# Kernel tuning notes

Hardware: AMD Instinct MI355X
Metric: run time of the kernel (lower is better)

The kernel has to match this reference:

```python
import jax, jax.numpy as jnp
import numpy as np
from jax import lax

N, L, C_IN, NOISE_C, COMP, NC = 256, 512, 514, 112, 16, 2
MAIN_IN = NOISE_C + COMP  # 128
FEAT = NC * 4 * L         # 4096

def _conv1d(x, w, b, pad):
    # x [N,C,L], w [O,I,K]
    y = lax.conv_general_dilated(x, w, (1,), [(pad, pad)], dimension_numbers=('NCH', 'OIH', 'NCH'))
    return y + b[None, :, None]

def _bn(x, g, b):
    # BatchNorm1d, training mode: biased batch stats over (N, L)
    m = x.mean(axis=(0, 2), keepdims=True)
    v = x.var(axis=(0, 2), keepdims=True)
    return (x - m) * lax.rsqrt(v + 1e-5) * g[None, :, None] + b[None, :, None]

def _lrelu(x):
    return jnp.where(x >= 0, x, 0.2 * x)

def _pos_encode(length, dim):
    j = np.arange(dim)
    div = 1.0 / np.power(10000.0, 2 * (j[:, None] // 2) / dim)   # [dim,1]
    ang = np.arange(length)[None, :] * div                       # [dim,length]
    ang = np.where((j % 2 == 0)[:, None], np.sin(ang), np.cos(ang))
    return jnp.asarray(ang[None], jnp.float32)                   # [1,dim,length]

def _assemble(circle_prob, slider_prob):
    # Vectorized run-length label expansion equivalent to the per-sample python while-loop.
    # circle_prob [N, L/2, 2], slider_prob [N, L/4, 2] -> [N, L, 3]
    n, B = slider_prob.shape[0], slider_prob.shape[1]
    c = jnp.argmax(circle_prob, -1)
    s = jnp.argmax(slider_prob, -1)
    zc = jnp.zeros(circle_prob.shape[:-1] + (1,), circle_prob.dtype)
    zs = jnp.zeros(slider_prob.shape[:-1] + (1,), slider_prob.dtype)
    cp3 = jnp.concatenate([circle_prob, zc], -1)                                   # insert 0 at class 2
    sp3 = jnp.concatenate([slider_prob[..., :1], zs, slider_prob[..., 1:]], -1)    # insert 0 at class 1
    pad100 = jnp.array([1., 0., 0.], cp3.dtype)
    pad001 = jnp.array([0., 0., 1.], cp3.dtype)
    bidx = jnp.arange(B)[None, :]
    # slider-body blocks: slider run continues and not cut by sequence end
    body = (s == 1) & (bidx < B - 1)
    prev_body = jnp.concatenate([jnp.zeros((n, 1), bool), body[:, :-1]], 1)
    # tail block ends a slider run (either run stops, or boundary block)
    tail = ((s == 1) & (bidx == B - 1)) | ((s == 0) & prev_body)
    # circle emission for each half-step: prob row if predicted circle else pad
    cr0 = jnp.where((c == 1)[..., None], cp3, pad100).reshape(n, B, 2, 3)
    bodyE = body[..., None]
    row0 = jnp.where((body | tail)[..., None], sp3, cr0[:, :, 0, :])
    row1 = jnp.where(bodyE, pad001, pad100)
    row2 = jnp.where(bodyE, pad001, cr0[:, :, 1, :])
    row3 = jnp.where(bodyE, pad001, pad100)
    return jnp.stack([row0, row1, row2, row3], 2).reshape(n, 4 * B, 3)

def _forward(noise, cond_data, gumbel_u, ext_w1, ext_b1, ext_w2, ext_b2, ext_bn_g, ext_bn_b,
             m_w1, m_b1, m_w2, m_b2, m_bn_g, m_bn_b, lin_w, lin_b, circ_w, circ_b, slid_w, slid_b):
    # FeatureExtractor
    x = cond_data.transpose(0, 2, 1)                      # [N, 514, L]
    x = _lrelu(_conv1d(x, ext_w1, ext_b1, 0))             # [N, 32, L]
    cond = _bn(_conv1d(x, ext_w2, ext_b2, 1), ext_bn_g, ext_bn_b)  # [N, 16, L]
    gen_in = jnp.concatenate([cond, noise.transpose(0, 2, 1)], 1) + _pos_encode(L, MAIN_IN)  # [N,128,L]
    h = _lrelu(_conv1d(gen_in, m_w1, m_b1, 3))            # [N, 32, L]
    h = _lrelu(_bn(_conv1d(h, m_w2, m_b2, 1), m_bn_g, m_bn_b))     # [N, 8, L]
    flat = _lrelu(h.reshape(h.shape[0], -1) @ lin_w + lin_b)       # [N, 4096]
    circle_prob = (flat @ circ_w + circ_b).reshape(-1, L // 2, NC)
    slider_prob = (flat @ slid_w + slid_b).reshape(-1, L // 4, NC)
    out = _assemble(circle_prob, slider_prob)             # [N, L, 3]
    # gumbel_softmax(hard=True, tau=1)
    g = -jnp.log(-jnp.log(gumbel_u + 1e-10) + 1e-10)
    logits = out + g
    y_soft = jax.nn.softmax(logits, -1)
    y_hard = jax.nn.one_hot(jnp.argmax(logits, -1), 3, dtype=y_soft.dtype)
    gen_out = y_hard + y_soft - lax.stop_gradient(y_soft)
    return gen_out, cond

def setup_inputs() -> dict:
    key = jax.random.key(0)
    ks = jax.random.split(key, 12)
    def rn(k, shape, fan_in):
        return jax.random.normal(k, shape, jnp.float32) * (1.0 / fan_in) ** 0.5
    return {
        'noise': jax.random.normal(ks[0], (N, L, NOISE_C), jnp.float32),
        'cond_data': jax.random.normal(ks[1], (N, L, C_IN), jnp.float32),
        'gumbel_u': jax.random.uniform(ks[2], (N, L, 3), jnp.float32),
        'ext_w1': rn(ks[3], (C_IN // 16, C_IN, 1), C_IN), 'ext_b1': jnp.zeros(C_IN // 16),
        'ext_w2': rn(ks[4], (COMP, C_IN // 16, 3), 3 * (C_IN // 16)), 'ext_b2': jnp.zeros(COMP),
        'ext_bn_g': jnp.ones(COMP), 'ext_bn_b': jnp.zeros(COMP),
        'm_w1': rn(ks[5], (NC * 16, MAIN_IN, 7), 7 * MAIN_IN), 'm_b1': jnp.zeros(NC * 16),
        'm_w2': rn(ks[6], (NC * 4, NC * 16, 3), 3 * NC * 16), 'm_b2': jnp.zeros(NC * 4),
        'm_bn_g': jnp.ones(NC * 4), 'm_bn_b': jnp.zeros(NC * 4),
        'lin_w': rn(ks[7], (FEAT, FEAT), FEAT), 'lin_b': jnp.zeros(FEAT),
        'circ_w': rn(ks[8], (FEAT, NC * L // 2), FEAT), 'circ_b': jnp.zeros(NC * L // 2),
        'slid_w': rn(ks[9], (FEAT, NC * L // 4), FEAT), 'slid_b': jnp.zeros(NC * L // 4),
    }

def reference(noise, cond_data, gumbel_u, ext_w1, ext_b1, ext_w2, ext_b2, ext_bn_g, ext_bn_b,
              m_w1, m_b1, m_w2, m_b2, m_bn_g, m_bn_b, lin_w, lin_b, circ_w, circ_b, slid_w, slid_b):
    return _forward(noise, cond_data, gumbel_u, ext_w1, ext_b1, ext_w2, ext_b2, ext_bn_g, ext_bn_b,
                    m_w1, m_b1, m_w2, m_b2, m_bn_g, m_bn_b, lin_w, lin_b, circ_w, circ_b, slid_w, slid_b)
```

## Files before the change

### kernel.cpp

```cpp
#include <hip/hip_runtime.h>
#include <math.h>

#define NB 256
#define LL 512
#define CIN 514

__device__ __forceinline__ float lrelu(float x) { return x >= 0.f ? x : 0.2f * x; }

__global__ __launch_bounds__(256) void k_pos(float* __restrict__ pos) {
    int idx = blockIdx.x * 256 + threadIdx.x;
    int c = idx >> 9, l = idx & 511;
    double e = (double)(2 * (c >> 1)) / 128.0;
    double dv = 1.0 / pow(10000.0, e);
    double a = (double)l * dv;
    pos[idx] = (float)((c & 1) ? cos(a) : sin(a));
}

__global__ __launch_bounds__(256) void k_posconv(const float* __restrict__ POS, const float* __restrict__ W,
                                                 const float* __restrict__ bias, float* __restrict__ PC) {
    const int t = threadIdx.x;
    const int o = blockIdx.x >> 4, l0 = (blockIdx.x & 15) * 32;
    const int l = l0 + (t & 31), cs = t >> 5;
    float acc = 0.f;
    for (int ci = 0; ci < 16; ++ci) {
        int c = cs * 16 + ci;
        float wv[7];
#pragma unroll
        for (int k = 0; k < 7; ++k) wv[k] = W[o * 896 + c * 7 + k];
#pragma unroll
        for (int k = 0; k < 7; ++k) {
            int gl = l + k - 3;
            if (gl >= 0 && gl < LL) acc += wv[k] * POS[c * LL + gl];
        }
    }
    __shared__ float red[8][33];
    red[cs][t & 31] = acc;
    __syncthreads();
    if (cs == 0) {
        float s = bias[o];
#pragma unroll
        for (int j = 0; j < 8; ++j) s += red[j][t & 31];
        PC[o * LL + l0 + (t & 31)] = s;
    }
}

__global__ __launch_bounds__(256) void k_conv1(const float* __restrict__ X, const float* __restrict__ W,
                                               const float* __restrict__ bias, float* __restrict__ out) {
    __shared__ __align__(16) float As[32][260];
    __shared__ __align__(16) float Bs[32][32];
    const int t = threadIdx.x;
    const int pos0 = blockIdx.x * 256;
    const int tx = t & 31, ty = t >> 5;
    const int rl = t >> 4, kp = t & 15;
    float acc[8][4];
#pragma unroll
    for (int p = 0; p < 8; ++p)
#pragma unroll
        for (int q = 0; q < 4; ++q) acc[p][q] = 0.f;

    for (int k0 = 0; k0 < CIN; k0 += 32) {
#pragma unroll
        for (int pass = 0; pass < 16; ++pass) {
            int row = pass * 16 + rl;
            int kk = kp * 2, gk = k0 + kk;
            float vx = 0.f, vy = 0.f;
            if (gk + 1 < CIN) {
                float2 v = *reinterpret_cast<const float2*>(X + (size_t)(pos0 + row) * CIN + gk);
                vx = v.x; vy = v.y;
            } else if (gk < CIN) {
                vx = X[(size_t)(pos0 + row) * CIN + gk];
            }
            As[kk][row] = vx;
            As[kk + 1][row] = vy;
        }
        {
            int o = t & 31, kg = t >> 5;
#pragma unroll
            for (int j = 0; j < 4; ++j) {
                int kk = kg * 4 + j, gk = k0 + kk;
                Bs[kk][o] = (gk < CIN) ? W[o * CIN + gk] : 0.f;
            }
        }
        __syncthreads();
#pragma unroll 8
        for (int kk = 0; kk < 32; ++kk) {
            float4 a0 = *reinterpret_cast<const float4*>(&As[kk][tx * 4]);
            float4 a1 = *reinterpret_cast<const float4*>(&As[kk][128 + tx * 4]);
            float4 b  = *reinterpret_cast<const float4*>(&Bs[kk][ty * 4]);
            float av[8] = {a0.x,a0.y,a0.z,a0.w,a1.x,a1.y,a1.z,a1.w};
            float bv[4] = {b.x,b.y,b.z,b.w};
#pragma unroll
            for (int p = 0; p < 8; ++p)
#pragma unroll
                for (int q = 0; q < 4; ++q) acc[p][q] += av[p] * bv[q];
        }
        __syncthreads();
    }
    const int n = pos0 >> 9, l0 = pos0 & 511;
#pragma unroll
    for (int q = 0; q < 4; ++q) {
        int o = ty * 4 + q;
        float bb = bias[o];
#pragma unroll
        for (int h = 0; h < 2; ++h) {
            float4 v;
            v.x = lrelu(acc[h*4+0][q] + bb);
            v.y = lrelu(acc[h*4+1][q] + bb);
            v.z = lrelu(acc[h*4+2][q] + bb);
            v.w = lrelu(acc[h*4+3][q] + bb);
            *reinterpret_cast<float4*>(out + ((size_t)n * 32 + o) * LL + l0 + h * 128 + tx * 4) = v;
        }
    }
}

__global__ __launch_bounds__(256) void k_conv2(const float* __restrict__ X, const float* __restrict__ W,
                                               const float* __restrict__ bias, float* __restrict__ out) {
    __shared__ __align__(16) float Xs[32][264];
    __shared__ __align__(16) float Ws[16][32][4];
    const int t = threadIdx.x;
    const int n = blockIdx.x >> 1, l0 = (blockIdx.x & 1) * 256;
    for (int idx = t; idx < 32 * 258; idx += 256) {
        int i = idx / 258, j = idx % 258;
        int gl = l0 - 1 + j;
        Xs[i][j] = (gl >= 0 && gl < LL) ? X[((size_t)n * 32 + i) * LL + gl] : 0.f;
    }
    for (int idx = t; idx < 1536; idx += 256) {
        int o = idx / 96, r = idx % 96;
        Ws[o][r / 3][r % 3] = W[idx];
    }
    __syncthreads();
    const int tx = t & 31, ty = t >> 5;
    float acc[2][8];
#pragma unroll
    for (int q = 0; q < 2; ++q)
#pragma unroll
        for (int p = 0; p < 8; ++p) acc[q][p] = 0.f;
    for (int i = 0; i < 32; ++i) {
        float4 a0 = *(const float4*)&Xs[i][tx*8];
        float4 a1 = *(const float4*)&Xs[i][tx*8+4];
        float4 a2 = *(const float4*)&Xs[i][tx*8+8];
        float a[12] = {a0.x,a0.y,a0.z,a0.w,a1.x,a1.y,a1.z,a1.w,a2.x,a2.y,a2.z,a2.w};
#pragma unroll
        for (int q = 0; q < 2; ++q) {
            float4 b = *(const float4*)&Ws[ty*2+q][i][0];
#pragma unroll
            for (int p = 0; p < 8; ++p)
                acc[q][p] += a[p]*b.x + a[p+1]*b.y + a[p+2]*b.z;
        }
    }
#pragma unroll
    for (int q = 0; q < 2; ++q) {
        int o = ty*2+q; float bb = bias[o];
#pragma unroll
        for (int h = 0; h < 2; ++h) {
            float4 v;
            v.x = acc[q][h*4+0] + bb; v.y = acc[q][h*4+1] + bb;
            v.z = acc[q][h*4+2] + bb; v.w = acc[q][h*4+3] + bb;
            *(float4*)(out + ((size_t)n*16 + o)*LL + l0 + tx*8 + h*4) = v;
        }
    }
}

__global__ __launch_bounds__(256) void k_redstats(const float* __restrict__ src, int C, float* __restrict__ part) {
    const int ch = blockIdx.x, sl = blockIdx.y, t = threadIdx.x;
    float s = 0.f, q = 0.f;
    for (int i = t; i < 4096; i += 256) {
        int n = sl*8 + (i >> 9), l = i & 511;
        float v = src[((size_t)n*C + ch)*LL + l];
        s += v; q += v*v;
    }
    __shared__ float rs[256], rq[256];
    rs[t] = s; rq[t] = q;
    __syncthreads();
    for (int off = 128; off > 0; off >>= 1) {
        if (t < off) { rs[t] += rs[t+off]; rq[t] += rq[t+off]; }
        __syncthreads();
    }
    if (t == 0) { part[(ch*32+sl)*2] = rs[0]; part[(ch*32+sl)*2+1] = rq[0]; }
}

__global__ void k_bnfinal(const float* __restrict__ part, const float* __restrict__ g,
                          const float* __restrict__ b, int C, float* __restrict__ ss) {
    int ch = threadIdx.x;
    if (ch >= C) return;
    float s = 0.f, q = 0.f;
    for (int j = 0; j < 32; ++j) { s += part[(ch*32 + j)*2]; q += part[(ch*32 + j)*2 + 1]; }
    float mean = s * (1.f/131072.f);
    float var = q * (1.f/131072.f) - mean*mean;
    float sc = g[ch] / sqrtf(var + 1e-5f);
    ss[ch] = sc;
    ss[C + ch] = b[ch] - mean * sc;
}

__global__ __launch_bounds__(256) void k_bnapply(const float* __restrict__ src, const float* __restrict__ ss,
        int C, float* __restrict__ dst, int act, int total4) {
    int i4 = blockIdx.x * 256 + threadIdx.x;
    if (i4 >= total4) return;
    int i = i4 << 2;
    int ch = (i >> 9) % C;
    float sc = ss[ch], sh = ss[C + ch];
    float4 v = reinterpret_cast<const float4*>(src)[i4];
    v.x = v.x*sc + sh; v.y = v.y*sc + sh; v.z = v.z*sc + sh; v.w = v.w*sc + sh;
    if (act) { v.x = lrelu(v.x); v.y = lrelu(v.y); v.z = lrelu(v.z); v.w = lrelu(v.w); }
    reinterpret_cast<float4*>(dst)[i4] = v;
}

__global__ __launch_bounds__(256) void k_mconv1(const float* __restrict__ C16, const float* __restrict__ NZ,
        const float* __restrict__ PC, const float* __restrict__ W,
        float* __restrict__ out0, float* __restrict__ out1) {
    __shared__ __align__(16) float Gs[16][264];
    __shared__ __align__(16) float Ws[32][16][8];
    const int t = threadIdx.x;
    const int n = blockIdx.x >> 2, l0 = ((blockIdx.x >> 1) & 1) * 256, z = blockIdx.x & 1;
    const int tx = t & 31, ty = t >> 5;
    float acc[4][8];
#pragma unroll
    for (int q = 0; q < 4; ++q)
#pragma unroll
        for (int p = 0; p < 8; ++p) acc[q][p] = 0.f;

    for (int cc = 0; cc < 4; ++cc) {
        const int ctg = z * 4 + cc;
        if (cc) __syncthreads();
        if (ctg == 0) {
            for (int idx = t; idx < 16*262; idx += 256) {
                int c = idx / 262, j = idx - c * 262;
                int gl = l0 - 3 + j;
                float v = 0.f;
                if (gl >= 0 && gl < LL) v = C16[((size_t)n*16 + c)*LL + gl];
                Gs[c][j] = v;
            }
        } else {
            int nc0 = ctg * 16 - 16;
            for (int idx = t; idx < 16*262; idx += 256) {
                int c = idx & 15, j = idx >> 4;
                int gl = l0 - 3 + j;
                float v = 0.f;
                if (gl >= 0 && gl < LL) v = NZ[((size_t)n*LL + gl)*112 + nc0 + c];
                Gs[c][j] = v;
            }
        }
        for (int idx = t; idx < 32*112; idx += 256) {
            int o = idx / 112, r = idx % 112;
            Ws[o][r / 7][r % 7] = W[(size_t)o*896 + ctg*112 + r];
        }
        __syncthreads();
        for (int ci = 0; ci < 16; ++ci) {
            float4 a0 = *(const float4*)&Gs[ci][tx*4];
            float4 a1 = *(const float4*)&Gs[ci][tx*4+4];
            float4 a2 = *(const float4*)&Gs[ci][tx*4+8];
            float4 a3 = *(const float4*)&Gs[ci][128+tx*4];
            float4 a4 = *(const float4*)&Gs[ci][128+tx*4+4];
            float4 a5 = *(const float4*)&Gs[ci][128+tx*4+8];
            float aA[12] = {a0.x,a0.y,a0.z,a0.w,a1.x,a1.y,a1.z,a1.w,a2.x,a2.y,a2.z,a2.w};
            float aB[12] = {a3.x,a3.y,a3.z,a3.w,a4.x,a4.y,a4.z,a4.w,a5.x,a5.y,a5.z,a5.w};
#pragma unroll
            for (int q = 0; q < 4; ++q) {
                float4 b0 = *(const float4*)&Ws[ty*4+q][ci][0];
                float4 b1 = *(const float4*)&Ws[ty*4+q][ci][4];
                float b[7] = {b0.x,b0.y,b0.z,b0.w,b1.x,b1.y,b1.z};
#pragma unroll
                for (int p = 0; p < 4; ++p) {
#pragma unroll
                    for (int k = 0; k < 7; ++k) {
                        acc[q][p]   += aA[p+k]*b[k];
                        acc[q][4+p] += aB[p+k]*b[k];
                    }
                }
            }
        }
    }
    float* out = z ? out1 : out0;
#pragma unroll
    for (int q = 0; q < 4; ++q) {
        int o = ty*4 + q;
        float4 p0 = {0.f,0.f,0.f,0.f}, p1 = {0.f,0.f,0.f,0.f};
        if (z == 0) {
            p0 = *(const float4*)(PC + o*LL + l0 + tx*4);
            p1 = *(const float4*)(PC + o*LL + l0 + 128 + tx*4);
        }
        float4 v0 = {acc[q][0]+p0.x, acc[q][1]+p0.y, acc[q][2]+p0.z, acc[q][3]+p0.w};
        float4 v1 = {acc[q][4]+p1.x, acc[q][5]+p1.y, acc[q][6]+p1.z, acc[q][7]+p1.w};
        *(float4*)(out + ((size_t)n*32 + o)*LL + l0 + tx*4) = v0;
        *(float4*)(out + ((size_t)n*32 + o)*LL + l0 + 128 + tx*4) = v1;
    }
}

__global__ __launch_bounds__(256) void k_mconv2(const float* __restrict__ P0, const float* __restrict__ P1,
        const float* __restrict__ W, const float* __restrict__ bias, float* __restrict__ out) {
    __shared__ __align__(16) float Xs[32][264];
    __shared__ __align__(16) float Ws[8][32][4];
    const int t = threadIdx.x;
    const int n = blockIdx.x >> 1, l0 = (blockIdx.x & 1) * 256;
    for (int idx = t; idx < 32 * 258; idx += 256) {
        int i = idx / 258, j = idx % 258;
        int gl = l0 - 1 + j;
        float v = 0.f;
        if (gl >= 0 && gl < LL) {
            size_t off = ((size_t)n * 32 + i) * LL + gl;
            v = lrelu(P0[off] + P1[off]);
        }
        Xs[i][j] = v;
    }
    for (int idx = t; idx < 768; idx += 256) {
        int o = idx / 96, r = idx % 96;
        Ws[o][r / 3][r % 3] = W[idx];
    }
    __syncthreads();
    const int tx = t & 31, ty = t >> 5;
    float acc[8];
#pragma unroll
    for (int p = 0; p < 8; ++p) acc[p] = 0.f;
    for (int i = 0; i < 32; ++i) {
        float4 a0 = *(const float4*)&Xs[i][tx*8];
        float4 a1 = *(const float4*)&Xs[i][tx*8+4];
        float4 a2 = *(const float4*)&Xs[i][tx*8+8];
        float a[12] = {a0.x,a0.y,a0.z,a0.w,a1.x,a1.y,a1.z,a1.w,a2.x,a2.y,a2.z,a2.w};
        float4 b = *(const float4*)&Ws[ty][i][0];
#pragma unroll
        for (int p = 0; p < 8; ++p)
            acc[p] += a[p]*b.x + a[p+1]*b.y + a[p+2]*b.z;
    }
    float bb = bias[ty];
#pragma unroll
    for (int h = 0; h < 2; ++h) {
        float4 v;
        v.x = acc[h*4+0] + bb; v.y = acc[h*4+1] + bb;
        v.z = acc[h*4+2] + bb; v.w = acc[h*4+3] + bb;
        *(float4*)(out + ((size_t)n*8 + ty)*LL + l0 + tx*8 + h*4) = v;
    }
}

__global__ __launch_bounds__(256) void k_lin(const float* __restrict__ A, const float* __restrict__ B,
                                             float* __restrict__ part) {
    __shared__ __align__(16) float As[32][36];
    __shared__ __align__(16) float Bs[32][132];
    const int t = threadIdx.x;
    const int m0 = blockIdx.x * 32, f0 = blockIdx.y * 128, z = blockIdx.z;
    const int tm = t & 7, tf = t >> 3;
    const int mi = t >> 3, kq = t & 7;
    float acc[4][4];
#pragma unroll
    for (int pm = 0; pm < 4; ++pm)
#pragma unroll
        for (int pf = 0; pf < 4; ++pf) acc[pm][pf] = 0.f;
    for (int k0 = z * 2048; k0 < z * 2048 + 2048; k0 += 32) {
        float4 av = *(const float4*)(A + (size_t)(m0 + mi) * 4096 + k0 + kq * 4);
        As[kq*4+0][mi] = av.x; As[kq*4+1][mi] = av.y; As[kq*4+2][mi] = av.z; As[kq*4+3][mi] = av.w;
#pragma unroll
        for (int pass = 0; pass < 4; ++pass) {
            int fi = pass * 32 + kq * 4;
            *(float4*)&Bs[mi][fi] = *(const float4*)(B + (size_t)(k0 + mi) * 4096 + f0 + fi);
        }
        __syncthreads();
#pragma unroll 8
        for (int kk = 0; kk < 32; ++kk) {
            float4 a = *(const float4*)&As[kk][tm * 4];
            float4 b = *(const float4*)&Bs[kk][tf * 4];
            float avv[4] = {a.x,a.y,a.z,a.w};
            float bvv[4] = {b.x,b.y,b.z,b.w};
#pragma unroll
            for (int pm = 0; pm < 4; ++pm)
#pragma unroll
                for (int pf = 0; pf < 4; ++pf) acc[pm][pf] += avv[pm]*bvv[pf];
        }
        __syncthreads();
    }
#pragma unroll
    for (int pm = 0; pm < 4; ++pm) {
        float4 v = {acc[pm][0], acc[pm][1], acc[pm][2], acc[pm][3]};
        *(float4*)(part + ((size_t)z * 256 + m0 + tm * 4 + pm) * 4096 + f0 + tf * 4) = v;
    }
}

__global__ __launch_bounds__(256) void k_linred(const float* __restrict__ part, const float* __restrict__ bias,
        float* __restrict__ out) {
    int i4 = blockIdx.x*256 + threadIdx.x;
    int i = i4 << 2;
    int f = i & 4095;
    float4 a = ((const float4*)part)[i4];
    float4 c = ((const float4*)(part + 1048576))[i4];
    float4 bb = *(const float4*)(bias + f);
    float4 r;
    r.x = lrelu(a.x + c.x + bb.x);
    r.y = lrelu(a.y + c.y + bb.y);
    r.z = lrelu(a.z + c.z + bb.z);
    r.w = lrelu(a.w + c.w + bb.w);
    ((float4*)out)[i4] = r;
}

__global__ __launch_bounds__(256) void k_heads(const float* __restrict__ A, const float* __restrict__ CW,
        const float* __restrict__ SW, float* __restrict__ part) {
    __shared__ __align__(16) float As[32][36];
    __shared__ __align__(16) float Bs[32][132];
    const int t = threadIdx.x;
    const int m0 = blockIdx.x * 32, f0 = blockIdx.y * 128, z = blockIdx.z;
    const float* B; int ldb, fb;
    if (f0 < 512) { B = CW; ldb = 512; fb = f0; } else { B = SW; ldb = 256; fb = f0 - 512; }
    const int tm = t & 7, tf = t >> 3;
    const int mi = t >> 3, kq = t & 7;
    float acc[4][4];
#pragma unroll
    for (int pm = 0; pm < 4; ++pm)
#pragma unroll
        for (int pf = 0; pf < 4; ++pf) acc[pm][pf] = 0.f;
    for (int k0 = z * 512; k0 < z * 512 + 512; k0 += 32) {
        float4 av = *(const float4*)(A + (size_t)(m0 + mi) * 4096 + k0 + kq * 4);
        As[kq*4+0][mi] = av.x; As[kq*4+1][mi] = av.y; As[kq*4+2][mi] = av.z; As[kq*4+3][mi] = av.w;
#pragma unroll
        for (int pass = 0; pass < 4; ++pass) {
            int fi = pass * 32 + kq * 4;
            *(float4*)&Bs[mi][fi] = *(const float4*)(B + (size_t)(k0 + mi) * ldb + fb + fi);
        }
        __syncthreads();
#pragma unroll 8
        for (int kk = 0; kk < 32; ++kk) {
            float4 a = *(const float4*)&As[kk][tm * 4];
            float4 b = *(const float4*)&Bs[kk][tf * 4];
            float avv[4] = {a.x,a.y,a.z,a.w};
            float bvv[4] = {b.x,b.y,b.z,b.w};
#pragma unroll
            for (int pm = 0; pm < 4; ++pm)
#pragma unroll
                for (int pf = 0; pf < 4; ++pf) acc[pm][pf] += avv[pm]*bvv[pf];
        }
        __syncthreads();
    }
#pragma unroll
    for (int pm = 0; pm < 4; ++pm) {
        float4 v = {acc[pm][0], acc[pm][1], acc[pm][2], acc[pm][3]};
        *(float4*)(part + ((size_t)z * 256 + m0 + tm * 4 + pm) * 768 + f0 + tf * 4) = v;
    }
}

__global__ __launch_bounds__(256) void k_headred(const float* __restrict__ part, const float* __restrict__ cb,
        const float* __restrict__ sb, float* __restrict__ circ, float* __restrict__ slid) {
    int i4 = blockIdx.x * 256 + threadIdx.x;
    int i = i4 << 2;
    int n = i / 768, f = i % 768;
    float4 s = {0.f,0.f,0.f,0.f};
#pragma unroll
    for (int ks = 0; ks < 8; ++ks) {
        float4 p = *(const float4*)(part + ((size_t)ks*256 + n)*768 + f);
        s.x += p.x; s.y += p.y; s.z += p.z; s.w += p.w;
    }
    if (f < 512) {
        float4 bb = *(const float4*)(cb + f);
        s.x += bb.x; s.y += bb.y; s.z += bb.z; s.w += bb.w;
        *(float4*)(circ + (size_t)n*512 + f) = s;
    } else {
        float4 bb = *(const float4*)(sb + f - 512);
        s.x += bb.x; s.y += bb.y; s.z += bb.z; s.w += bb.w;
        *(float4*)(slid + (size_t)n*256 + f - 512) = s;
    }
}

__global__ __launch_bounds__(128) void k_assemble(const float* __restrict__ circ, const float* __restrict__ slid,
        const float* __restrict__ gum, float* __restrict__ out) {
    const int n = blockIdx.x;
    const int b = threadIdx.x;
    const float* sp = slid + (size_t)n * 256;
    const float* cp = circ + (size_t)n * 512;
    float sl0 = sp[2*b], sl1 = sp[2*b+1];
    int s = sl1 > sl0 ? 1 : 0;
    int prevb = 0;
    if (b > 0) prevb = (sp[2*b-1] > sp[2*b-2]) ? 1 : 0;
    bool body = (s == 1) && (b < 127);
    bool tail = ((s == 1) && (b == 127)) || ((s == 0) && (prevb == 1));
    float c0a = cp[4*b], c0b = cp[4*b+1], c1a = cp[4*b+2], c1b = cp[4*b+3];
    bool cA = c0b > c0a, cB = c1b > c1a;
    float rows[4][3];
    if (body || tail)      { rows[0][0]=sl0; rows[0][1]=0.f; rows[0][2]=sl1; }
    else if (cA)           { rows[0][0]=c0a; rows[0][1]=c0b; rows[0][2]=0.f; }
    else                   { rows[0][0]=1.f; rows[0][1]=0.f; rows[0][2]=0.f; }
    if (body)              { rows[1][0]=0.f; rows[1][1]=0.f; rows[1][2]=1.f; }
    else                   { rows[1][0]=1.f; rows[1][1]=0.f; rows[1][2]=0.f; }
    if (body)              { rows[2][0]=0.f; rows[2][1]=0.f; rows[2][2]=1.f; }
    else if (cB)           { rows[2][0]=c1a; rows[2][1]=c1b; rows[2][2]=0.f; }
    else                   { rows[2][0]=1.f; rows[2][1]=0.f; rows[2][2]=0.f; }
    rows[3][0]=rows[1][0]; rows[3][1]=rows[1][1]; rows[3][2]=rows[1][2];
#pragma unroll
    for (int r = 0; r < 4; ++r) {
        int l = 4*b + r;
        const float* u = gum + ((size_t)n*512 + l)*3;
        float g0 = -logf(-logf(u[0]+1e-10f)+1e-10f);
        float g1 = -logf(-logf(u[1]+1e-10f)+1e-10f);
        float g2 = -logf(-logf(u[2]+1e-10f)+1e-10f);
        float t0 = rows[r][0]+g0, t1 = rows[r][1]+g1, t2 = rows[r][2]+g2;
        int am = 0; float mv = t0;
        if (t1 > mv) { am = 1; mv = t1; }
        if (t2 > mv) { am = 2; mv = t2; }
        float e0 = expf(t0-mv), e1 = expf(t1-mv), e2 = expf(t2-mv);
        float ssum = e0+e1+e2;
        float y0 = e0/ssum, y1 = e1/ssum, y2 = e2/ssum;
        float* o = out + ((size_t)n*512 + l)*3;
        o[0] = ((am==0?1.f:0.f) + y0) - y0;
        o[1] = ((am==1?1.f:0.f) + y1) - y1;
        o[2] = ((am==2?1.f:0.f) + y2) - y2;
    }
}

extern "C" void kernel_launch(void* const* d_in, const int* in_sizes, int n_in,
                              void* d_out, int out_size, void* d_ws, size_t ws_size,
                              hipStream_t stream) {
    const float* noise   = (const float*)d_in[0];
    const float* cond    = (const float*)d_in[1];
    const float* gumbel  = (const float*)d_in[2];
    const float* ext_w1  = (const float*)d_in[3];
    const float* ext_b1  = (const float*)d_in[4];
    const float* ext_w2  = (const float*)d_in[5];
    const float* ext_b2  = (const float*)d_in[6];
    const float* ext_bng = (const float*)d_in[7];
    const float* ext_bnb = (const float*)d_in[8];
    const float* m_w1    = (const float*)d_in[9];
    const float* m_b1    = (const float*)d_in[10];
    const float* m_w2    = (const float*)d_in[11];
    const float* m_b2    = (const float*)d_in[12];
    const float* m_bng   = (const float*)d_in[13];
    const float* m_bnb   = (const float*)d_in[14];
    const float* lin_w   = (const float*)d_in[15];
    const float* lin_b   = (const float*)d_in[16];
    const float* circ_w  = (const float*)d_in[17];
    const float* circ_b  = (const float*)d_in[18];
    const float* slid_w  = (const float*)d_in[19];
    const float* slid_b  = (const float*)d_in[20];

    float* genout  = (float*)d_out;
    float* condout = (float*)d_out + 256*512*3;

    float* w     = (float*)d_ws;
    float* x1    = w;
    float* y2    = x1 + 4194304;
    float* posb  = y2 + 2097152;
    float* circ  = posb + 65536;
    float* slid  = circ + 131072;
    float* flatB = slid + 65536;
    float* partL = flatB + 1048576;
    float* partH = partL + 2097152;
    float* stats = partH + 1572864;
    float* pc    = stats + 4096;
    float* buf1  = flatB;

    k_pos<<<256, 256, 0, stream>>>(posb);
    k_posconv<<<512, 256, 0, stream>>>(posb, m_w1, m_b1, pc);
    k_conv1<<<512, 256, 0, stream>>>(cond, ext_w1, ext_b1, x1);
    k_conv2<<<512, 256, 0, stream>>>(x1, ext_w2, ext_b2, y2);
    k_redstats<<<dim3(16,32), 256, 0, stream>>>(y2, 16, stats);
    k_bnfinal<<<1, 64, 0, stream>>>(stats, ext_bng, ext_bnb, 16, stats + 2048);
    k_bnapply<<<2048, 256, 0, stream>>>(y2, stats + 2048, 16, condout, 0, 524288);
    k_mconv1<<<1024, 256, 0, stream>>>(condout, noise, pc, m_w1, x1, buf1);
    k_mconv2<<<512, 256, 0, stream>>>(x1, buf1, m_w2, m_b2, y2);
    k_redstats<<<dim3(8,32), 256, 0, stream>>>(y2, 8, stats);
    k_bnfinal<<<1, 64, 0, stream>>>(stats, m_bng, m_bnb, 8, stats + 2048 + 64);
    k_bnapply<<<1024, 256, 0, stream>>>(y2, stats + 2048 + 64, 8, y2, 1, 262144);
    k_lin<<<dim3(8,32,2), 256, 0, stream>>>(y2, lin_w, partL);
    k_linred<<<1024, 256, 0, stream>>>(partL, lin_b, flatB);
    k_heads<<<dim3(8,6,8), 256, 0, stream>>>(flatB, circ_w, slid_w, partH);
    k_headred<<<192, 256, 0, stream>>>(partH, circ_b, slid_b, circ, slid);
    k_assemble<<<256, 128, 0, stream>>>(circ, slid, gumbel, genout);
}
```

Before: 588.1 us.

## Split conv1 K across two blocks with register-prefetched double buffering

Result: faster. 550.1 us (-6.5%).

```diff
diff --git a/kernel.cpp b/kernel.cpp
--- a/kernel.cpp
+++ b/kernel.cpp
@@ -45,75 +45,122 @@
 }
 
 __global__ __launch_bounds__(256) void k_conv1(const float* __restrict__ X, const float* __restrict__ W,
-                                               const float* __restrict__ bias, float* __restrict__ out) {
-    __shared__ __align__(16) float As[32][260];
-    __shared__ __align__(16) float Bs[32][32];
+                                               float* __restrict__ P0, float* __restrict__ P1) {
+    __shared__ __align__(16) float As[16][524];
+    __shared__ __align__(16) float Bs[16][36];
     const int t = threadIdx.x;
-    const int pos0 = blockIdx.x * 256;
-    const int tx = t & 31, ty = t >> 5;
-    const int rl = t >> 4, kp = t & 15;
-    float acc[8][4];
-#pragma unroll
-    for (int p = 0; p < 8; ++p)
-#pragma unroll
-        for (int q = 0; q < 4; ++q) acc[p][q] = 0.f;
-
-    for (int k0 = 0; k0 < CIN; k0 += 32) {
-#pragma unroll
-        for (int pass = 0; pass < 16; ++pass) {
-            int row = pass * 16 + rl;
-            int kk = kp * 2, gk = k0 + kk;
-            float vx = 0.f, vy = 0.f;
-            if (gk + 1 < CIN) {
-                float2 v = *reinterpret_cast<const float2*>(X + (size_t)(pos0 + row) * CIN + gk);
-                vx = v.x; vy = v.y;
-            } else if (gk < CIN) {
-                vx = X[(size_t)(pos0 + row) * CIN + gk];
+    const int n = blockIdx.x >> 1, z = blockIdx.x & 1;
+    const int kbase = z * 256;
+    const int nch = z ? 17 : 16;
+    const int tl = t & 63, to = t >> 6;
+    const size_t rowbase = (size_t)n * 512 * CIN;
+
+    float acc[8][8];
+#pragma unroll
+    for (int oi = 0; oi < 8; ++oi)
+#pragma unroll
+        for (int p = 0; p < 8; ++p) acc[oi][p] = 0.f;
+
+    float2 pf[16];
+    float2 pfb;
+
+    {
+        const int kb = kbase;
+#pragma unroll
+        for (int ps = 0; ps < 16; ++ps) {
+            int idx = ps * 256 + t;
+            int pos = idx >> 3, kp = idx & 7;
+            int gk = kb + kp * 2;
+            float2 v = {0.f, 0.f};
+            if (gk + 1 < CIN) v = *(const float2*)(X + rowbase + (size_t)pos * CIN + gk);
+            else if (gk < CIN) v.x = X[rowbase + (size_t)pos * CIN + gk];
+            pf[ps] = v;
+        }
+        {
+            int o = t >> 3, kp = t & 7;
+            int gk = kb + kp * 2;
+            float2 v = {0.f, 0.f};
+            if (gk + 1 < CIN) v = *(const float2*)(W + (size_t)o * CIN + gk);
+            else if (gk < CIN) v.x = W[(size_t)o * CIN + gk];
+            pfb = v;
+        }
+#pragma unroll
+        for (int ps = 0; ps < 16; ++ps) {
+            int idx = ps * 256 + t;
+            int pos = idx >> 3, kp = idx & 7;
+            As[kp * 2][pos] = pf[ps].x;
+            As[kp * 2 + 1][pos] = pf[ps].y;
+        }
+        {
+            int o = t >> 3, kp = t & 7;
+            Bs[kp * 2][o] = pfb.x;
+            Bs[kp * 2 + 1][o] = pfb.y;
+        }
+    }
+    __syncthreads();
+
+    for (int c = 0; c < nch; ++c) {
+        if (c + 1 < nch) {
+            const int kb = kbase + (c + 1) * 16;
+#pragma unroll
+            for (int ps = 0; ps < 16; ++ps) {
+                int idx = ps * 256 + t;
+                int pos = idx >> 3, kp = idx & 7;
+                int gk = kb + kp * 2;
+                float2 v = {0.f, 0.f};
+                if (gk + 1 < CIN) v = *(const float2*)(X + rowbase + (size_t)pos * CIN + gk);
+                else if (gk < CIN) v.x = X[rowbase + (size_t)pos * CIN + gk];
+                pf[ps] = v;
             }
-            As[kk][row] = vx;
-            As[kk + 1][row] = vy;
-        }
-        {
-            int o = t & 31, kg = t >> 5;
-#pragma unroll
-            for (int j = 0; j < 4; ++j) {
-                int kk = kg * 4 + j, gk = k0 + kk;
-                Bs[kk][o] = (gk < CIN) ? W[o * CIN + gk] : 0.f;
+            int o = t >> 3, kp = t & 7;
+            int gk = kb + kp * 2;
+            float2 v = {0.f, 0.f};
+            if (gk + 1 < CIN) v = *(const float2*)(W + (size_t)o * CIN + gk);
+            else if (gk < CIN) v.x = W[(size_t)o * CIN + gk];
+            pfb = v;
+        }
+#pragma unroll
+        for (int kk = 0; kk < 16; ++kk) {
+            float4 aL = *(const float4*)&As[kk][tl * 4];
+            float4 aH = *(const float4*)&As[kk][256 + tl * 4];
+            float4 b0 = *(const float4*)&Bs[kk][to * 8];
+            float4 b1 = *(const float4*)&Bs[kk][to * 8 + 4];
+            float av[8] = {aL.x, aL.y, aL.z, aL.w, aH.x, aH.y, aH.z, aH.w};
+            float bv[8] = {b0.x, b0.y, b0.z, b0.w, b1.x, b1.y, b1.z, b1.w};
+#pragma unroll
+            for (int oi = 0; oi < 8; ++oi)
+#pragma unroll
+                for (int p = 0; p < 8; ++p) acc[oi][p] += av[p] * bv[oi];
+        }
+        __syncthreads();
+        if (c + 1 < nch) {
+#pragma unroll
+            for (int ps = 0; ps < 16; ++ps) {
+                int idx = ps * 256 + t;
+                int pos = idx >> 3, kp = idx & 7;
+                As[kp * 2][pos] = pf[ps].x;
+                As[kp * 2 + 1][pos] = pf[ps].y;
             }
-        }
-        __syncthreads();
-#pragma unroll 8
-        for (int kk = 0; kk < 32; ++kk) {
-            float4 a0 = *reinterpret_cast<const float4*>(&As[kk][tx * 4]);
-            float4 a1 = *reinterpret_cast<const float4*>(&As[kk][128 + tx * 4]);
-            float4 b  = *reinterpret_cast<const float4*>(&Bs[kk][ty * 4]);
-            float av[8] = {a0.x,a0.y,a0.z,a0.w,a1.x,a1.y,a1.z,a1.w};
-            float bv[4] = {b.x,b.y,b.z,b.w};
-#pragma unroll
-            for (int p = 0; p < 8; ++p)
-#pragma unroll
-                for (int q = 0; q < 4; ++q) acc[p][q] += av[p] * bv[q];
-        }
-        __syncthreads();
-    }
-    const int n = pos0 >> 9, l0 = pos0 & 511;
-#pragma unroll
-    for (int q = 0; q < 4; ++q) {
-        int o = ty * 4 + q;
-        float bb = bias[o];
-#pragma unroll
-        for (int h = 0; h < 2; ++h) {
-            float4 v;
-            v.x = lrelu(acc[h*4+0][q] + bb);
-            v.y = lrelu(acc[h*4+1][q] + bb);
-            v.z = lrelu(acc[h*4+2][q] + bb);
-            v.w = lrelu(acc[h*4+3][q] + bb);
-            *reinterpret_cast<float4*>(out + ((size_t)n * 32 + o) * LL + l0 + h * 128 + tx * 4) = v;
-        }
-    }
-}
-
-__global__ __launch_bounds__(256) void k_conv2(const float* __restrict__ X, const float* __restrict__ W,
+            int o = t >> 3, kp = t & 7;
+            Bs[kp * 2][o] = pfb.x;
+            Bs[kp * 2 + 1][o] = pfb.y;
+        }
+        __syncthreads();
+    }
+
+    float* P = z ? P1 : P0;
+#pragma unroll
+    for (int oi = 0; oi < 8; ++oi) {
+        int o = to * 8 + oi;
+        float4 v0 = {acc[oi][0], acc[oi][1], acc[oi][2], acc[oi][3]};
+        float4 v1 = {acc[oi][4], acc[oi][5], acc[oi][6], acc[oi][7]};
+        *(float4*)(P + ((size_t)n * 32 + o) * LL + tl * 4) = v0;
+        *(float4*)(P + ((size_t)n * 32 + o) * LL + 256 + tl * 4) = v1;
+    }
+}
+
+__global__ __launch_bounds__(256) void k_conv2(const float* __restrict__ P0, const float* __restrict__ P1,
+                                               const float* __restrict__ b1, const float* __restrict__ W,
                                                const float* __restrict__ bias, float* __restrict__ out) {
     __shared__ __align__(16) float Xs[32][264];
     __shared__ __align__(16) float Ws[16][32][4];
@@ -122,7 +169,12 @@
     for (int idx = t; idx < 32 * 258; idx += 256) {
         int i = idx / 258, j = idx % 258;
         int gl = l0 - 1 + j;
-        Xs[i][j] = (gl >= 0 && gl < LL) ? X[((size_t)n * 32 + i) * LL + gl] : 0.f;
+        float v = 0.f;
+        if (gl >= 0 && gl < LL) {
+            size_t off = ((size_t)n * 32 + i) * LL + gl;
+            v = lrelu(P0[off] + P1[off] + b1[i]);
+        }
+        Xs[i][j] = v;
     }
     for (int idx = t; idx < 1536; idx += 256) {
         int o = idx / 96, r = idx % 96;
@@ -543,8 +595,8 @@
 
     k_pos<<<256, 256, 0, stream>>>(posb);
     k_posconv<<<512, 256, 0, stream>>>(posb, m_w1, m_b1, pc);
-    k_conv1<<<512, 256, 0, stream>>>(cond, ext_w1, ext_b1, x1);
-    k_conv2<<<512, 256, 0, stream>>>(x1, ext_w2, ext_b2, y2);
+    k_conv1<<<512, 256, 0, stream>>>(cond, ext_w1, x1, buf1);
+    k_conv2<<<512, 256, 0, stream>>>(x1, buf1, ext_b1, ext_w2, ext_b2, y2);
     k_redstats<<<dim3(16,32), 256, 0, stream>>>(y2, 16, stats);
     k_bnfinal<<<1, 64, 0, stream>>>(stats, ext_bng, ext_bnb, 16, stats + 2048);
     k_bnapply<<<2048, 256, 0, stream>>>(y2, stats + 2048, 16, condout, 0, 524288);
```
